# Kernel tuning notes

Measured on AMD Instinct MI355X. Metric: run time of the kernel, lower is better.

Reference implementation:

```python
import jax, jax.numpy as jnp
import numpy as np

FRAME_SIZE = 80
PITCH_MIN = 32
PITCH_MAX = 300
RADIUS = 2


def setup_inputs() -> dict:
    key = jax.random.key(0)
    k1, k2 = jax.random.split(key)
    B, C, F = 64, 1, 4000
    x = jax.random.normal(k1, (B, C, FRAME_SIZE * F), dtype=jnp.float32)
    # valid period range so lookup indices stay in-bounds (p <= PITCH_MAX - RADIUS)
    periods = jax.random.randint(k2, (B, F), 0, 299)
    return {"x": x, "periods": periods}


def reference(x, periods):
    B, C, N = x.shape          # C must be 1 (as required by torch.gather in original)
    F = periods.shape[1]
    W = 2 * RADIUS + 1
    offs = jnp.arange(-RADIUS, RADIUS + 1)          # [W]
    idx = jnp.arange(N)                              # [N]
    # repeat_interleave(periods, frame_size, dim=1) -> per-sample period
    p_up = jnp.repeat(periods, FRAME_SIZE, axis=1)   # [B, N]
    lookup = idx[None, :] + PITCH_MAX - p_up         # [B, N]
    lookup = lookup[:, :, None] + offs               # [B, N, W]
    x_pad = jnp.pad(x, ((0, 0), (0, 0), (PITCH_MAX, 0)))  # [B, C, N+PITCH_MAX]
    xs = x_pad[:, 0, :]                              # [B, N+PITCH_MAX]
    # gather lagged samples (no materialization of the repeated x_ext tensor)
    x_select = xs[jnp.arange(B)[:, None, None], lookup]   # [B, N, W]
    x_frames = x.reshape(B, C, F, FRAME_SIZE, 1)
    lag_frames = x_select.reshape(B, 1, F, FRAME_SIZE, W)
    dotp = jnp.sum(x_frames * lag_frames, axis=-2)         # [B, C, F, W]
    frame_nrg = jnp.sum(x_frames * x_frames, axis=-2)      # [B, C, F, 1]
    lag_nrg = jnp.sum(lag_frames * lag_frames, axis=-2)    # [B, 1, F, W]
    acorr = dotp / jnp.sqrt(frame_nrg * lag_nrg + 1e-9)
    return acorr
```

## Files before the change

kernel.cpp:

```cpp
#include <hip/hip_runtime.h>

namespace {
constexpr int kFrame = 80;
constexpr int kRad   = 2;
constexpr int kW     = 5;
constexpr int kB     = 64;
constexpr int kF     = 4000;
constexpr int kN     = kFrame * kF;

constexpr int FPB   = 64;
constexpr int NBLK  = (kB * kF) / FPB;
constexpr int NXCD  = 8;
constexpr int CPX   = NBLK / NXCD;
}

__device__ __forceinline__ float qsum(float v) {
    v += __int_as_float(__builtin_amdgcn_mov_dpp(__float_as_int(v), 0xB1, 0xF, 0xF, true));
    v += __int_as_float(__builtin_amdgcn_mov_dpp(__float_as_int(v), 0x4E, 0xF, 0xF, true));
    return v;
}

__device__ __forceinline__ float4 ld4c(const float* __restrict__ xb, int g) {
    float t0 = (g + 0 >= 0) ? xb[min(g + 0, kN - 1)] : 0.f;
    float t1 = (g + 1 >= 0) ? xb[min(g + 1, kN - 1)] : 0.f;
    float t2 = (g + 2 >= 0) ? xb[min(g + 2, kN - 1)] : 0.f;
    float t3 = (g + 3 >= 0) ? xb[min(g + 3, kN - 1)] : 0.f;
    return make_float4(t0, t1, t2, t3);
}

__global__ __launch_bounds__(256, 4)
void pitch_acorr_kernel(const float* __restrict__ x,
                        const int* __restrict__ periods,
                        float* __restrict__ out) {
    const int bid = blockIdx.x;
    const int wid = (bid & (NXCD - 1)) * CPX + (bid >> 3);
    const int tid = threadIdx.x;
    const int fl  = tid >> 2;
    const int q   = tid & 3;
    const int h   = q * 20;

    const int gf = wid * FPB + fl;
    const int b  = gf / kF;
    const int f  = gf - b * kF;
    const float* xb = x + (long long)b * kN;

    const int p = periods[gf];

    const int fst = f * kFrame + h;
    const float4 Fa = *reinterpret_cast<const float4*>(xb + fst +  0);
    const float4 Fb = *reinterpret_cast<const float4*>(xb + fst +  4);
    const float4 Fc = *reinterpret_cast<const float4*>(xb + fst +  8);
    const float4 Fd = *reinterpret_cast<const float4*>(xb + fst + 12);
    const float4 Fe = *reinterpret_cast<const float4*>(xb + fst + 16);

    const int lbase = f * kFrame - p - kRad;
    const int s     = lbase & 3;
    const int A0    = lbase - s;
    const int gst   = A0 + h;

    float4 Ga, Gb, Gc, Gd, Ge, Gf_, Gg;
    const bool safe = (A0 >= 0) && (A0 + 88 <= kN);
    if (safe) {
        Ga = *reinterpret_cast<const float4*>(xb + gst +  0);
        Gb = *reinterpret_cast<const float4*>(xb + gst +  4);
        Gc = *reinterpret_cast<const float4*>(xb + gst +  8);
        Gd = *reinterpret_cast<const float4*>(xb + gst + 12);
        Ge = *reinterpret_cast<const float4*>(xb + gst + 16);
        Gf_= *reinterpret_cast<const float4*>(xb + gst + 20);
        Gg = *reinterpret_cast<const float4*>(xb + gst + 24);
    } else {
        Ga = ld4c(xb, gst +  0);
        Gb = ld4c(xb, gst +  4);
        Gc = ld4c(xb, gst +  8);
        Gd = ld4c(xb, gst + 12);
        Ge = ld4c(xb, gst + 16);
        Gf_= ld4c(xb, gst + 20);
        Gg = ld4c(xb, gst + 24);
    }

    const float g0 = Ga.x, g1 = Ga.y, g2 = Ga.z, g3 = Ga.w,
                g4 = Gb.x, g5 = Gb.y, g6 = Gb.z, g7 = Gb.w,
                g8 = Gc.x, g9 = Gc.y, g10 = Gc.z, g11 = Gc.w,
                g12 = Gd.x, g13 = Gd.y, g14 = Gd.z, g15 = Gd.w,
                g16 = Ge.x, g17 = Ge.y, g18 = Ge.z, g19 = Ge.w,
                g20 = Gf_.x, g21 = Gf_.y, g22 = Gf_.z, g23 = Gf_.w,
                g24 = Gg.x, g25 = Gg.y, g26 = Gg.z;

    const float E0 = g0*g0 + g1*g1 + g2*g2 + g3*g3 + g4*g4 + g5*g5 + g6*g6
                   + g7*g7 + g8*g8 + g9*g9 + g10*g10 + g11*g11 + g12*g12
                   + g13*g13 + g14*g14 + g15*g15 + g16*g16 + g17*g17 + g18*g18
                   + g19*g19;

    float fn = 0.f;
    float D0 = 0.f, D1 = 0.f, D2 = 0.f, D3 = 0.f,
          D4 = 0.f, D5 = 0.f, D6 = 0.f, D7 = 0.f;

#define STEP(FT, A, B, C, D, E, F, G, H)                                       \
    { const float ft = (FT);                                                   \
      fn += ft * ft;                                                           \
      D0 += ft * (A); D1 += ft * (B); D2 += ft * (C); D3 += ft * (D);          \
      D4 += ft * (E); D5 += ft * (F); D6 += ft * (G); D7 += ft * (H); }

    STEP(Fa.x, g0, g1, g2, g3, g4, g5, g6, g7)
    STEP(Fa.y, g1, g2, g3, g4, g5, g6, g7, g8)
    STEP(Fa.z, g2, g3, g4, g5, g6, g7, g8, g9)
    STEP(Fa.w, g3, g4, g5, g6, g7, g8, g9, g10)
    STEP(Fb.x, g4, g5, g6, g7, g8, g9, g10, g11)
    STEP(Fb.y, g5, g6, g7, g8, g9, g10, g11, g12)
    STEP(Fb.z, g6, g7, g8, g9, g10, g11, g12, g13)
    STEP(Fb.w, g7, g8, g9, g10, g11, g12, g13, g14)
    STEP(Fc.x, g8, g9, g10, g11, g12, g13, g14, g15)
    STEP(Fc.y, g9, g10, g11, g12, g13, g14, g15, g16)
    STEP(Fc.z, g10, g11, g12, g13, g14, g15, g16, g17)
    STEP(Fc.w, g11, g12, g13, g14, g15, g16, g17, g18)
    STEP(Fd.x, g12, g13, g14, g15, g16, g17, g18, g19)
    STEP(Fd.y, g13, g14, g15, g16, g17, g18, g19, g20)
    STEP(Fd.z, g14, g15, g16, g17, g18, g19, g20, g21)
    STEP(Fd.w, g15, g16, g17, g18, g19, g20, g21, g22)
    STEP(Fe.x, g16, g17, g18, g19, g20, g21, g22, g23)
    STEP(Fe.y, g17, g18, g19, g20, g21, g22, g23, g24)
    STEP(Fe.z, g18, g19, g20, g21, g22, g23, g24, g25)
    STEP(Fe.w, g19, g20, g21, g22, g23, g24, g25, g26)
#undef STEP

    const float E1 = E0 + (g20*g20 - g0*g0);
    const float E2 = E1 + (g21*g21 - g1*g1);
    const float E3 = E2 + (g22*g22 - g2*g2);
    const float E4 = E3 + (g23*g23 - g3*g3);
    const float E5 = E4 + (g24*g24 - g4*g4);
    const float E6 = E5 + (g25*g25 - g5*g5);
    const float E7 = E6 + (g26*g26 - g6*g6);

    const bool s1 = (s & 1) != 0, s2 = (s & 2) != 0;
    float d0 = s2 ? (s1 ? D3 : D2) : (s1 ? D1 : D0);
    float d1 = s2 ? (s1 ? D4 : D3) : (s1 ? D2 : D1);
    float d2 = s2 ? (s1 ? D5 : D4) : (s1 ? D3 : D2);
    float d3 = s2 ? (s1 ? D6 : D5) : (s1 ? D4 : D3);
    float d4 = s2 ? (s1 ? D7 : D6) : (s1 ? D5 : D4);
    float e0 = s2 ? (s1 ? E3 : E2) : (s1 ? E1 : E0);
    float e1 = s2 ? (s1 ? E4 : E3) : (s1 ? E2 : E1);
    float e2 = s2 ? (s1 ? E5 : E4) : (s1 ? E3 : E2);
    float e3 = s2 ? (s1 ? E6 : E5) : (s1 ? E4 : E3);
    float e4 = s2 ? (s1 ? E7 : E6) : (s1 ? E5 : E4);

    fn = qsum(fn);
    d0 = qsum(d0); d1 = qsum(d1); d2 = qsum(d2); d3 = qsum(d3); d4 = qsum(d4);
    e0 = qsum(e0); e1 = qsum(e1); e2 = qsum(e2); e3 = qsum(e3); e4 = qsum(e4);

    float* op = out + (long long)gf * kW;
    const float dq = (q & 2) ? ((q & 1) ? d3 : d2) : ((q & 1) ? d1 : d0);
    const float eq = (q & 2) ? ((q & 1) ? e3 : e2) : ((q & 1) ? e1 : e0);
    op[q] = dq * rsqrtf(fn * eq + 1e-9f);
    if (q == 0) op[4] = d4 * rsqrtf(fn * e4 + 1e-9f);
}

extern "C" void kernel_launch(void* const* d_in, const int* in_sizes, int n_in,
                              void* d_out, int out_size, void* d_ws, size_t ws_size,
                              hipStream_t stream) {
    const float* x       = (const float*)d_in[0];
    const int*   periods = (const int*)d_in[1];
    float*       out     = (float*)d_out;

    pitch_acorr_kernel<<<NBLK, 256, 0, stream>>>(x, periods, out);
}
```

Before: 20.53 us.

## Stage per-wave input slab with halo in LDS for lag window reads

Each wavefront cooperatively loads a contiguous slab covering its 16 frames plus a 320-sample lookback halo into LDS using coalesced float4 loads. Frame and lagged windows are then read from LDS through a padded address mapping that avoids bank conflicts. This replaces scattered, misaligned-per-thread global gathers with coalesced loads. The cost is redundant halo traffic (about a third extra), LDS usage that limits occupancy, and extra register staging.

```diff
diff --git a/kernel.cpp b/kernel.cpp
--- a/kernel.cpp
+++ b/kernel.cpp
@@ -8,10 +8,23 @@
 constexpr int kF     = 4000;
 constexpr int kN     = kFrame * kF;
 
-constexpr int FPB   = 64;
-constexpr int NBLK  = (kB * kF) / FPB;
-constexpr int NXCD  = 8;
-constexpr int CPX   = NBLK / NXCD;
+constexpr int FPW  = 16;
+constexpr int WPB  = 4;
+constexpr int NBLK = (kB * kF) / (FPW * WPB);
+constexpr int GPB  = kF / FPW;
+
+constexpr int HALO_LO = 320;
+constexpr int HALO_HI = 84;
+constexpr int LNW  = HALO_LO + FPW * kFrame + HALO_HI;
+constexpr int SLAB = LNW + 4 * ((LNW + 79) / 80);
+constexpr int NQW  = (LNW / 4 + 63) / 64;
+
+constexpr int NXCD = 8, CPX = NBLK / NXCD;
+}
+
+__device__ __forceinline__ int ldsPhys(int L) {
+    int row = ((L >> 4) * 103) >> 9;
+    return L + (row << 2);
 }
 
 __device__ __forceinline__ float qsum(float v) {
@@ -20,63 +33,78 @@
     return v;
 }
 
-__device__ __forceinline__ float4 ld4c(const float* __restrict__ xb, int g) {
-    float t0 = (g + 0 >= 0) ? xb[min(g + 0, kN - 1)] : 0.f;
-    float t1 = (g + 1 >= 0) ? xb[min(g + 1, kN - 1)] : 0.f;
-    float t2 = (g + 2 >= 0) ? xb[min(g + 2, kN - 1)] : 0.f;
-    float t3 = (g + 3 >= 0) ? xb[min(g + 3, kN - 1)] : 0.f;
-    return make_float4(t0, t1, t2, t3);
-}
-
 __global__ __launch_bounds__(256, 4)
 void pitch_acorr_kernel(const float* __restrict__ x,
                         const int* __restrict__ periods,
                         float* __restrict__ out) {
-    const int bid = blockIdx.x;
-    const int wid = (bid & (NXCD - 1)) * CPX + (bid >> 3);
-    const int tid = threadIdx.x;
-    const int fl  = tid >> 2;
-    const int q   = tid & 3;
-    const int h   = q * 20;
+    __shared__ float lds[WPB * SLAB];
 
-    const int gf = wid * FPB + fl;
-    const int b  = gf / kF;
-    const int f  = gf - b * kF;
+    const int bid  = blockIdx.x;
+    const int wid  = (bid & (NXCD - 1)) * CPX + (bid >> 3);
+    const int tid  = threadIdx.x;
+    const int w    = tid >> 6;
+    const int lane = tid & 63;
+    const int fl   = lane >> 2;
+    const int q    = lane & 3;
+    const int h    = q * 20;
+    float* __restrict__ slab = &lds[w * SLAB];
+
+    const int ws = wid * WPB + w;
+    const int b  = ws / GPB;
+    const int f0 = (ws - b * GPB) * FPW;
     const float* xb = x + (long long)b * kN;
+    const int o  = f0 * kFrame - HALO_LO;
 
-    const int p = periods[gf];
+    const int gf = ws * FPW + fl;
+    const int p  = periods[gf];
 
-    const int fst = f * kFrame + h;
-    const float4 Fa = *reinterpret_cast<const float4*>(xb + fst +  0);
-    const float4 Fb = *reinterpret_cast<const float4*>(xb + fst +  4);
-    const float4 Fc = *reinterpret_cast<const float4*>(xb + fst +  8);
-    const float4 Fd = *reinterpret_cast<const float4*>(xb + fst + 12);
-    const float4 Fe = *reinterpret_cast<const float4*>(xb + fst + 16);
+    float4 r[NQW];
+    const bool safe = (o >= 0) && (o + LNW <= kN);
+    if (safe) {
+#pragma unroll
+        for (int k = 0; k < NQW; ++k) {
+            int i4 = (k * 64 + lane) * 4;
+            if (i4 < LNW) r[k] = *reinterpret_cast<const float4*>(xb + o + i4);
+        }
+    } else {
+#pragma unroll
+        for (int k = 0; k < NQW; ++k) {
+            int i4 = (k * 64 + lane) * 4;
+            if (i4 < LNW) {
+                int g = o + i4;
+                float t0 = (g + 0 >= 0) ? xb[min(g + 0, kN - 1)] : 0.f;
+                float t1 = (g + 1 >= 0) ? xb[min(g + 1, kN - 1)] : 0.f;
+                float t2 = (g + 2 >= 0) ? xb[min(g + 2, kN - 1)] : 0.f;
+                float t3 = (g + 3 >= 0) ? xb[min(g + 3, kN - 1)] : 0.f;
+                r[k] = make_float4(t0, t1, t2, t3);
+            }
+        }
+    }
+#pragma unroll
+    for (int k = 0; k < NQW; ++k) {
+        int i4 = (k * 64 + lane) * 4;
+        if (i4 < LNW)
+            *reinterpret_cast<float4*>(&slab[ldsPhys(i4)]) = r[k];
+    }
 
-    const int lbase = f * kFrame - p - kRad;
+    const int fbase = HALO_LO + fl * kFrame;
+    const int lbase = fbase - p - kRad;
     const int s     = lbase & 3;
     const int A0    = lbase - s;
     const int gst   = A0 + h;
+    const int fst   = fbase + h;
+    const int fph   = fst + ((4 + fl) << 2);
 
-    float4 Ga, Gb, Gc, Gd, Ge, Gf_, Gg;
-    const bool safe = (A0 >= 0) && (A0 + 88 <= kN);
-    if (safe) {
-        Ga = *reinterpret_cast<const float4*>(xb + gst +  0);
-        Gb = *reinterpret_cast<const float4*>(xb + gst +  4);
-        Gc = *reinterpret_cast<const float4*>(xb + gst +  8);
-        Gd = *reinterpret_cast<const float4*>(xb + gst + 12);
-        Ge = *reinterpret_cast<const float4*>(xb + gst + 16);
-        Gf_= *reinterpret_cast<const float4*>(xb + gst + 20);
-        Gg = *reinterpret_cast<const float4*>(xb + gst + 24);
-    } else {
-        Ga = ld4c(xb, gst +  0);
-        Gb = ld4c(xb, gst +  4);
-        Gc = ld4c(xb, gst +  8);
-        Gd = ld4c(xb, gst + 12);
-        Ge = ld4c(xb, gst + 16);
-        Gf_= ld4c(xb, gst + 20);
-        Gg = ld4c(xb, gst + 24);
-    }
+    const float4 Fa = *reinterpret_cast<const float4*>(&slab[fph +  0]);
+    const float4 Fb = *reinterpret_cast<const float4*>(&slab[fph +  4]);
+    const float4 Fc = *reinterpret_cast<const float4*>(&slab[fph +  8]);
+    const float4 Fd = *reinterpret_cast<const float4*>(&slab[fph + 12]);
+    const float4 Fe = *reinterpret_cast<const float4*>(&slab[fph + 16]);
+
+#define GQ(u) (*reinterpret_cast<const float4*>(&slab[ldsPhys(gst + 4 * (u))]))
+    const float4 Ga = GQ(0), Gb = GQ(1), Gc = GQ(2), Gd = GQ(3),
+                 Ge = GQ(4), Gf_ = GQ(5), Gg = GQ(6);
+#undef GQ
 
     const float g0 = Ga.x, g1 = Ga.y, g2 = Ga.z, g3 = Ga.w,
                 g4 = Gb.x, g5 = Gb.y, g6 = Gb.z, g7 = Gb.w,
```

New measurement: 20.35 us. Within noise of the previous version (-0.8%).
